# Kernel tuning notes

Measured on AMD Instinct MI355X. Metric: run time of the kernel, lower is better.

Reference implementation:

```python
import jax, jax.numpy as jnp
import numpy as np
from functools import partial

TAU_MEM = 10.0
TAU_SYN = (5.0, 10.0)
THRESHOLD = 1.0
WINDOW = 0.3
BATCH = 32
T = 256
N_SYN = 2
N_NEURONS = 2048


@jax.custom_vjp
def spike_fn(v_shifted):
    # Heaviside of (vmem - threshold); surrogate gradient is a boxcar of width `window`.
    return (v_shifted > 0).astype(v_shifted.dtype)


def _spike_fwd(v_shifted):
    return spike_fn(v_shifted), v_shifted


def _spike_bwd(v_shifted, g):
    surr = (jnp.abs(v_shifted) < WINDOW).astype(g.dtype) / WINDOW
    return (g * surr,)


spike_fn.defvjp(_spike_fwd, _spike_bwd)


def setup_inputs() -> dict:
    key = jax.random.key(0)
    # Poisson-like analog spike input, shape (batch*T, n_syn, n_neurons)
    binary_input = (jax.random.uniform(key, (BATCH * T, N_SYN, N_NEURONS), dtype=jnp.float32) < 0.1
                    ).astype(jnp.float32)
    return {"binary_input": binary_input}


def reference(binary_input):
    # (B*T, n_syn, N) -> (B, T, n_syn, N) -> time-major, synapse-last: (T, B, N, n_syn)
    x = binary_input.reshape(BATCH, T, N_SYN, N_NEURONS).transpose(1, 0, 3, 2)

    alpha_mem = jnp.exp(jnp.float32(-1.0 / TAU_MEM))
    alpha_syn = jnp.exp(-1.0 / jnp.asarray(TAU_SYN, dtype=jnp.float32))  # [n_syn]

    def step(carry, inp_t):
        vmem, isyn = carry                      # vmem [B,N], isyn [B,N,n_syn]
        isyn = alpha_syn * isyn + inp_t         # leaky synaptic integration
        vmem = alpha_mem * vmem + isyn.sum(-1)  # leaky membrane integration
        spikes = spike_fn(vmem - THRESHOLD)     # threshold crossing
        vmem = vmem - spikes * THRESHOLD        # reset by subtraction
        return (vmem, isyn), spikes

    v0 = jnp.zeros((BATCH, N_NEURONS), dtype=x.dtype)
    i0 = jnp.zeros((BATCH, N_NEURONS, N_SYN), dtype=x.dtype)
    _, all_spikes = jax.lax.scan(step, (v0, i0), x)  # [T, B, N]

    # back to (batch*T, N) as in the torch module's trailing reshape
    return all_spikes.transpose(1, 0, 2).reshape(-1, N_NEURONS)
```

## Files before the change

kernel.cpp:

```cpp
#include <hip/hip_runtime.h>
#include <math.h>

#define T_STEPS   256
#define N_NEUR    2048
#define N_BATCH   32

__global__ __launch_bounds__(256) void snn_scan_kernel(
    const float* __restrict__ in,
    float* __restrict__ out,
    float a_mem, float a_s0, float a_s1)
{
    const int tid = blockIdx.x * blockDim.x + threadIdx.x;
    const int n = tid & (N_NEUR - 1);
    const int b = tid >> 11;

    const float* pin = in + (size_t)b * T_STEPS * 2 * N_NEUR + n;
    float* pout      = out + (size_t)b * T_STEPS * N_NEUR + n;

    float vmem = 0.0f;
    float i0 = 0.0f;
    float i1 = 0.0f;

    #pragma unroll 8
    for (int t = 0; t < T_STEPS; ++t) {
        const float x0 = pin[(size_t)t * (2 * N_NEUR)];
        const float x1 = pin[(size_t)t * (2 * N_NEUR) + N_NEUR];

        i0 = __fadd_rn(__fmul_rn(a_s0, i0), x0);
        i1 = __fadd_rn(__fmul_rn(a_s1, i1), x1);

        const float ssum = __fadd_rn(i0, i1);
        vmem = __fadd_rn(__fmul_rn(a_mem, vmem), ssum);

        const float vs = __fsub_rn(vmem, 1.0f);
        const bool fired = (vs > 0.0f);
        const float spike = fired ? 1.0f : 0.0f;
        vmem = fired ? vs : vmem;

        pout[(size_t)t * N_NEUR] = spike;
    }
}

extern "C" void kernel_launch(void* const* d_in, const int* in_sizes, int n_in,
                              void* d_out, int out_size, void* d_ws, size_t ws_size,
                              hipStream_t stream) {
    const float* in = (const float*)d_in[0];
    float* out = (float*)d_out;

    const float a_s0  = (float)exp((double)(-1.0f / 5.0f));
    const float a_s1  = (float)exp((double)(-1.0f / 10.0f));
    const float a_mem = (float)exp((double)(-1.0f / 10.0f));

    const int total_threads = N_BATCH * N_NEUR;
    dim3 block(256);
    dim3 grid(total_threads / 256);

    snn_scan_kernel<<<grid, block, 0, stream>>>(in, out, a_mem, a_s0, a_s1);
}
```

Baseline: 209.6 us.

## Software-pipeline input loads with a register ring and use nontemporal loads/stores

Replaces the unrolled per-step loads with a 16-deep register prefetch ring, so each block of 16 timesteps issues the loads for the next block while it computes the current one. This keeps more memory requests in flight per thread to hide latency in what is a bandwidth-bound sequential scan. Loads and stores also become nontemporal to avoid polluting the cache with streamed data. The cost is about 32 extra live registers per thread, which may lower occupancy.

```diff
diff --git a/kernel.cpp b/kernel.cpp
--- a/kernel.cpp
+++ b/kernel.cpp
@@ -10,34 +10,53 @@
     float* __restrict__ out,
     float a_mem, float a_s0, float a_s1)
 {
+    constexpr int D = 16;
+    constexpr int STRIDE = 2 * N_NEUR;
+
     const int tid = blockIdx.x * blockDim.x + threadIdx.x;
     const int n = tid & (N_NEUR - 1);
     const int b = tid >> 11;
 
-    const float* pin = in + (size_t)b * T_STEPS * 2 * N_NEUR + n;
+    const float* pin = in + (size_t)b * T_STEPS * STRIDE + n;
     float* pout      = out + (size_t)b * T_STEPS * N_NEUR + n;
 
-    float vmem = 0.0f;
-    float i0 = 0.0f;
-    float i1 = 0.0f;
+    float xa[D], xb[D];
 
-    #pragma unroll 8
-    for (int t = 0; t < T_STEPS; ++t) {
-        const float x0 = pin[(size_t)t * (2 * N_NEUR)];
-        const float x1 = pin[(size_t)t * (2 * N_NEUR) + N_NEUR];
+    #pragma unroll
+    for (int j = 0; j < D; ++j) {
+        xa[j] = __builtin_nontemporal_load(&pin[j * STRIDE]);
+        xb[j] = __builtin_nontemporal_load(&pin[j * STRIDE + N_NEUR]);
+    }
 
-        i0 = __fadd_rn(__fmul_rn(a_s0, i0), x0);
-        i1 = __fadd_rn(__fmul_rn(a_s1, i1), x1);
+    float vmem = 0.0f, i0 = 0.0f, i1 = 0.0f;
 
-        const float ssum = __fadd_rn(i0, i1);
-        vmem = __fadd_rn(__fmul_rn(a_mem, vmem), ssum);
+    #pragma unroll 1
+    for (int blk = 0; blk < T_STEPS / D; ++blk) {
+        const int tbase = blk * D;
+        const bool pf = (blk + 1) < (T_STEPS / D);
+        #pragma unroll
+        for (int j = 0; j < D; ++j) {
+            const float x0 = xa[j];
+            const float x1 = xb[j];
 
-        const float vs = __fsub_rn(vmem, 1.0f);
-        const bool fired = (vs > 0.0f);
-        const float spike = fired ? 1.0f : 0.0f;
-        vmem = fired ? vs : vmem;
+            if (pf) {
+                const int tf = tbase + D + j;
+                xa[j] = __builtin_nontemporal_load(&pin[tf * STRIDE]);
+                xb[j] = __builtin_nontemporal_load(&pin[tf * STRIDE + N_NEUR]);
+            }
 
-        pout[(size_t)t * N_NEUR] = spike;
+            i0 = __fadd_rn(__fmul_rn(a_s0, i0), x0);
+            i1 = __fadd_rn(__fmul_rn(a_s1, i1), x1);
+
+            const float ssum = __fadd_rn(i0, i1);
+            vmem = __fadd_rn(__fmul_rn(a_mem, vmem), ssum);
+
+            const float vs = __fsub_rn(vmem, 1.0f);
+            const bool fired = (vs > 0.0f);
+            __builtin_nontemporal_store(fired ? 1.0f : 0.0f,
+                                        &pout[(tbase + j) * N_NEUR]);
+            vmem = fired ? vs : vmem;
+        }
     }
 }
 
```

Measured after the change: 303.3 us. 44.7% more time.

## Double-buffer input timesteps into LDS with async 16-byte global loads

Applied to the files above, without the earlier changes.

Each block handles 256 neurons of one batch and stages 16-timestep tiles of input into LDS with asynchronous global-to-LDS 16-byte copies. The copies are double-buffered so the next tile is fetched while the current tile's recurrence runs. This replaces one dependent scalar strided load per timestep per thread, which left the sequential scan latency-bound, with wide loads and prefetching. The cost is 64KB of LDS per block, which limits occupancy, a block barrier per tile, and reliance on the compiler inserting the right wait counts for the async loads.

```diff
diff --git a/kernel.cpp b/kernel.cpp
--- a/kernel.cpp
+++ b/kernel.cpp
@@ -1,43 +1,79 @@
 #include <hip/hip_runtime.h>
 #include <math.h>
 
-#define T_STEPS   256
-#define N_NEUR    2048
-#define N_BATCH   32
+#define T_STEPS 256
+#define N_NEUR  2048
+#define N_BATCH 32
+#define STRIDE  (2 * N_NEUR)
+
+#define TT      16
+#define NTILE   (T_STEPS / TT)
+#define BN      256
+
+__device__ __forceinline__ void async_cp16(const float* g, float* l) {
+    __builtin_amdgcn_global_load_lds(
+        (const __attribute__((address_space(1))) void*)g,
+        (__attribute__((address_space(3))) void*)l,
+        16, 0, 0);
+}
 
 __global__ __launch_bounds__(256) void snn_scan_kernel(
     const float* __restrict__ in,
     float* __restrict__ out,
     float a_mem, float a_s0, float a_s1)
 {
-    const int tid = blockIdx.x * blockDim.x + threadIdx.x;
-    const int n = tid & (N_NEUR - 1);
-    const int b = tid >> 11;
+    __shared__ float buf[2][TT * 2 * BN];
 
-    const float* pin = in + (size_t)b * T_STEPS * 2 * N_NEUR + n;
-    float* pout      = out + (size_t)b * T_STEPS * N_NEUR + n;
+    const int tid = threadIdx.x;
+    const int bid = blockIdx.x;
+    const int b   = bid >> 3;
+    const int n0  = (bid & 7) << 8;
 
-    float vmem = 0.0f;
-    float i0 = 0.0f;
-    float i1 = 0.0f;
+    const float* gin = in + (size_t)b * T_STEPS * STRIDE + n0;
+    float* pout      = out + (size_t)b * T_STEPS * N_NEUR + n0 + tid;
 
-    #pragma unroll 8
-    for (int t = 0; t < T_STEPS; ++t) {
-        const float x0 = pin[(size_t)t * (2 * N_NEUR)];
-        const float x1 = pin[(size_t)t * (2 * N_NEUR) + N_NEUR];
+    const int toff = (tid >> 7) * STRIDE + ((tid >> 6) & 1) * N_NEUR + (tid & 63) * 4;
+    const int ldsf = tid * 4;
 
-        i0 = __fadd_rn(__fmul_rn(a_s0, i0), x0);
-        i1 = __fadd_rn(__fmul_rn(a_s1, i1), x1);
+    #pragma unroll
+    for (int j = 0; j < TT / 2; ++j) {
+        async_cp16(gin + (size_t)(2 * j) * STRIDE + toff, &buf[0][j * 1024 + ldsf]);
+    }
+    __syncthreads();
 
-        const float ssum = __fadd_rn(i0, i1);
-        vmem = __fadd_rn(__fmul_rn(a_mem, vmem), ssum);
+    float vmem = 0.0f, i0 = 0.0f, i1 = 0.0f;
 
-        const float vs = __fsub_rn(vmem, 1.0f);
-        const bool fired = (vs > 0.0f);
-        const float spike = fired ? 1.0f : 0.0f;
-        vmem = fired ? vs : vmem;
+    #pragma unroll
+    for (int k = 0; k < NTILE; ++k) {
+        if (k + 1 < NTILE) {
+            const float* gt = gin + (size_t)(k + 1) * TT * STRIDE + toff;
+            float* lb = &buf[(k + 1) & 1][0];
+            #pragma unroll
+            for (int j = 0; j < TT / 2; ++j) {
+                async_cp16(gt + (size_t)(2 * j) * STRIDE, lb + j * 1024 + ldsf);
+            }
+        }
 
-        pout[(size_t)t * N_NEUR] = spike;
+        const float* lb = &buf[k & 1][0];
+        float* po = pout + (size_t)k * TT * N_NEUR;
+
+        #pragma unroll
+        for (int t = 0; t < TT; ++t) {
+            const float x0 = lb[t * 512 + tid];
+            const float x1 = lb[t * 512 + 256 + tid];
+
+            i0 = __fadd_rn(__fmul_rn(a_s0, i0), x0);
+            i1 = __fadd_rn(__fmul_rn(a_s1, i1), x1);
+
+            const float ssum = __fadd_rn(i0, i1);
+            vmem = __fadd_rn(__fmul_rn(a_mem, vmem), ssum);
+
+            const float vs = __fsub_rn(vmem, 1.0f);
+            const bool fired = (vs > 0.0f);
+            po[(size_t)t * N_NEUR] = fired ? 1.0f : 0.0f;
+            vmem = fired ? vs : vmem;
+        }
+        __syncthreads();
     }
 }
 
@@ -51,9 +87,8 @@
     const float a_s1  = (float)exp((double)(-1.0f / 10.0f));
     const float a_mem = (float)exp((double)(-1.0f / 10.0f));
 
-    const int total_threads = N_BATCH * N_NEUR;
     dim3 block(256);
-    dim3 grid(total_threads / 256);
+    dim3 grid(N_BATCH * (N_NEUR / BN));
 
     snn_scan_kernel<<<grid, block, 0, stream>>>(in, out, a_mem, a_s0, a_s1);
 }
```

After: 209.8 us. Within noise of the previous version (+0.1%).
